# Optimization experiments

Hardware: AMD Instinct MI355X
Metric: run time of the kernel (lower is better)

The kernel has to match this reference:

```python
import jax, jax.numpy as jnp
import numpy as np

NU, NI, K, D, B = 100000, 50000, 100, 64, 8192


def setup_inputs() -> dict:
    key = jax.random.key(0)
    ks = jax.random.split(key, 16)
    s = lambda fan_in: np.sqrt(2.0 / fan_in)  # kaiming_normal-ish scale
    return {
        "user_emb": jax.random.normal(ks[0], (NU, D), jnp.float32) * s(D),
        "item_emb": jax.random.normal(ks[1], (NI, D), jnp.float32) * s(D),
        "user_scr_tensor": jax.random.uniform(ks[2], (NU, K), jnp.float32) / K,
        "item_scr_tensor": jax.random.uniform(ks[3], (NI, K), jnp.float32) / K,
        "w1": jax.random.normal(ks[4], (64, 128), jnp.float32) * s(128),
        "b1": jnp.zeros((64,), jnp.float32),
        "w2": jax.random.normal(ks[5], (64, 64), jnp.float32) * s(64),
        "b2": jnp.zeros((64,), jnp.float32),
        "w3": jax.random.normal(ks[6], (32, 64), jnp.float32) * s(64),
        "b3": jnp.zeros((32,), jnp.float32),
        "w4": jax.random.normal(ks[7], (32, 32), jnp.float32) * s(32),
        "b4": jnp.zeros((32,), jnp.float32),
        "w5": jax.random.normal(ks[8], (1, 32), jnp.float32) * s(32),
        "b5": jnp.zeros((1,), jnp.float32),
        "user_idx_tensor": jax.random.randint(ks[9], (NU, K), 0, NU, jnp.int32),
        "item_idx_tensor": jax.random.randint(ks[10], (NI, K), 0, NI, jnp.int32),
        "user_idxs": jax.random.randint(ks[11], (B,), 0, NU, jnp.int32),
        "item_idxs": jax.random.randint(ks[12], (B,), 0, NI, jnp.int32),
    }


def _scored_pool(idx_tensor, emb, scr, idxs):
    neighs = idx_tensor[idxs]          # [B, K]
    neigh_emb = emb[neighs]            # [B, K, D]
    neigh_scr = scr[neighs]            # [B, K, K]
    return jnp.einsum("bkj,bjd->bkd", neigh_scr, neigh_emb)


def reference(user_emb, item_emb, user_scr_tensor, item_scr_tensor,
              w1, b1, w2, b2, w3, b3, w4, b4, w5, b5,
              user_idx_tensor, item_idx_tensor, user_idxs, item_idxs):
    su = _scored_pool(user_idx_tensor, user_emb, user_scr_tensor, user_idxs)  # [B,K,D]
    si = _scored_pool(item_idx_tensor, item_emb, item_scr_tensor, item_idxs)  # [B,K,D]
    x = jnp.concatenate([su, si], axis=2)  # [B, K, 2D]
    x = jax.nn.relu(x @ w1.T + b1)
    x = jax.nn.relu(x @ w2.T + b2)
    x = jax.nn.relu(x @ w3.T + b3)
    x = jax.nn.relu(x @ w4.T + b4)
    x = jax.nn.sigmoid(x @ w5.T + b5)  # [B, K, 1]
    return jnp.mean(x, axis=-2).squeeze()  # [B]
```

## Files before the change

kernel.cpp:

```cpp
#include <hip/hip_runtime.h>
#include <hip/hip_bf16.h>
#include <math.h>

typedef __attribute__((ext_vector_type(8))) short short8;
typedef __attribute__((ext_vector_type(4))) float f32x4;

#define KN 100

#define W1_OFF 0
#define W2_OFF 8192
#define W3_OFF 12288
#define W4_OFF 14336
#define SCRU_OFF 16384
#define SCRI_OFF (SCRU_OFF + 100000 * 128)
#define EMBU_OFF (SCRI_OFF + 50000 * 128)
#define EMBI_OFF (EMBU_OFF + 100000 * 64)

#define ET_OFF 0
#define XU_OFF (64 * 136)
#define XI_OFF (XU_OFF + 112 * 72)
#define S_TOT  (XI_OFF + 112 * 72)

__device__ __forceinline__ unsigned short f2bf(float f) {
  __hip_bfloat16 h = __float2bfloat16(f);
  return __builtin_bit_cast(unsigned short, h);
}

__device__ __forceinline__ void st8(unsigned short* d, float4 a, float4 b) {
  short8 h;
  h[0] = (short)f2bf(a.x); h[1] = (short)f2bf(a.y);
  h[2] = (short)f2bf(a.z); h[3] = (short)f2bf(a.w);
  h[4] = (short)f2bf(b.x); h[5] = (short)f2bf(b.y);
  h[6] = (short)f2bf(b.z); h[7] = (short)f2bf(b.w);
  *reinterpret_cast<short8*>(d) = h;
}

__global__ void prep(const float* __restrict__ w1, const float* __restrict__ w2,
                     const float* __restrict__ w3, const float* __restrict__ w4,
                     const float* __restrict__ uscr, const float* __restrict__ iscr,
                     const float* __restrict__ uemb, const float* __restrict__ iemb,
                     unsigned short* __restrict__ ws) {
  int t = blockIdx.x * 256 + threadIdx.x;
  if (t < 15360) {
    const float* src; int rel, o, i, kt, base;
    if (t < 8192)       { src = w1; rel = t;         o = rel >> 7; i = rel & 127; kt = 4; base = W1_OFF; }
    else if (t < 12288) { src = w2; rel = t - 8192;  o = rel >> 6; i = rel & 63;  kt = 2; base = W2_OFF; }
    else if (t < 14336) { src = w3; rel = t - 12288; o = rel >> 6; i = rel & 63;  kt = 2; base = W3_OFF; }
    else                { src = w4; rel = t - 14336; o = rel >> 5; i = rel & 31;  kt = 1; base = W4_OFF; }
    int n = o >> 4, l15 = o & 15, k = i >> 5, quad = (i >> 3) & 3, j = i & 7;
    ws[base + ((n * kt + k) * 64 + quad * 16 + l15) * 8 + j] = f2bf(src[rel]);
    return;
  }
  int rel = t - 15360;
  const float4 z4 = {0.f, 0.f, 0.f, 0.f};
  if (rel < 2400000) {
    const float* src; unsigned short* dst; int row, g;
    if (rel < 1600000) {
      row = rel >> 4; g = rel & 15;
      src = uscr + (size_t)row * 100;
      dst = ws + SCRU_OFF + (size_t)row * 128 + g * 8;
    } else {
      int q = rel - 1600000; row = q >> 4; g = q & 15;
      src = iscr + (size_t)row * 100;
      dst = ws + SCRI_OFF + (size_t)row * 128 + g * 8;
    }
    float4 va = (g < 13) ? *reinterpret_cast<const float4*>(src + g * 8) : z4;
    float4 vb = (g < 12) ? *reinterpret_cast<const float4*>(src + g * 8 + 4) : z4;
    st8(dst, va, vb);
    return;
  }
  rel -= 2400000;
  if (rel < 1200000) {
    const float* src; unsigned short* dst; int row, g;
    if (rel < 800000) {
      row = rel >> 3; g = rel & 7;
      src = uemb + (size_t)row * 64;
      dst = ws + EMBU_OFF + (size_t)row * 64 + g * 8;
    } else {
      int q = rel - 800000; row = q >> 3; g = q & 7;
      src = iemb + (size_t)row * 64;
      dst = ws + EMBI_OFF + (size_t)row * 64 + g * 8;
    }
    float4 va = *reinterpret_cast<const float4*>(src + g * 8);
    float4 vb = *reinterpret_cast<const float4*>(src + g * 8 + 4);
    st8(dst, va, vb);
  }
}

template <int NT, int KT, bool RELU>
__device__ __forceinline__ void mlp_layer(const short8* a,
                                          const unsigned short* __restrict__ gw,
                                          const float* __restrict__ bias,
                                          unsigned short* __restrict__ Y, int sY,
                                          int w, int l15, int quad, int lane) {
#pragma unroll
  for (int n = 0; n < NT; ++n) {
    f32x4 acc = {0.f, 0.f, 0.f, 0.f};
#pragma unroll
    for (int k = 0; k < KT; ++k) {
      short8 bf = *reinterpret_cast<const short8*>(gw + ((n * KT + k) * 64 + lane) * 8);
      acc = __builtin_amdgcn_mfma_f32_16x16x32_bf16(a[k], bf, acc, 0, 0, 0);
    }
    const int col = n * 16 + l15;
    const float bv = bias[col];
#pragma unroll
    for (int r = 0; r < 4; ++r) {
      float v = acc[r] + bv;
      if (RELU) v = fmaxf(v, 0.f);
      Y[(w * 16 + quad * 4 + r) * sY + col] = f2bf(v);
    }
  }
}

__launch_bounds__(448)
__global__ void cnn_mfma3(
    const unsigned short* __restrict__ ws,
    const float* __restrict__ b1, const float* __restrict__ b2,
    const float* __restrict__ b3, const float* __restrict__ b4,
    const float* __restrict__ w5, const float* __restrict__ b5,
    const int* __restrict__ user_idx_t, const int* __restrict__ item_idx_t,
    const int* __restrict__ user_idxs, const int* __restrict__ item_idxs,
    float* __restrict__ out) {
  __shared__ __align__(16) unsigned short S[S_TOT];
  __shared__ int s_nb[2][112];
  __shared__ float s_red[7];

  const int b = blockIdx.x;
  const int tid = threadIdx.x;
  const int w = tid >> 6;
  const int lane = tid & 63;
  const int l15 = lane & 15, quad = lane >> 4;

  if (tid < 112) {
    s_nb[0][tid] = (tid < KN) ? user_idx_t[(size_t)user_idxs[b] * KN + tid] : 0;
  } else if (tid >= 128 && tid < 240) {
    int i = tid - 128;
    s_nb[1][i] = (i < KN) ? item_idx_t[(size_t)item_idxs[b] * KN + i] : 0;
  }
  {
    int* z = (int*)S;
    for (int i = tid; i < (64 * 136) / 2; i += 448) z[i] = 0;
  }
  __syncthreads();

  const int mrow = w * 16 + l15;
  const int c = lane & 31, half = lane >> 5;

#pragma unroll 1
  for (int src = 0; src < 2; ++src) {
    const unsigned short* scrb = ws + (src ? SCRI_OFF : SCRU_OFF);
    const unsigned short* embb = ws + (src ? EMBI_OFF : EMBU_OFF);
    const int* nb = s_nb[src];

    short8 a[4];
    {
      const unsigned short* arow = scrb + (size_t)nb[mrow] * 128;
#pragma unroll
      for (int k = 0; k < 4; ++k)
        a[k] = *reinterpret_cast<const short8*>(arow + k * 32 + quad * 8);
    }

#pragma unroll
    for (int rr = 0; rr < 8; ++rr) {
      const int rbase = w + rr * 7;
      if (rbase < 50) {
        const int r = rbase * 2 + half;
        unsigned int v = *reinterpret_cast<const unsigned int*>(
            embb + (size_t)nb[r] * 64 + c * 2);
        S[ET_OFF + (2 * c) * 136 + r] = (unsigned short)(v & 0xffffu);
        S[ET_OFF + (2 * c + 1) * 136 + r] = (unsigned short)(v >> 16);
      }
    }
    __syncthreads();

    const int xoff = src ? XI_OFF : XU_OFF;
#pragma unroll
    for (int n = 0; n < 4; ++n) {
      f32x4 acc = {0.f, 0.f, 0.f, 0.f};
#pragma unroll
      for (int k = 0; k < 4; ++k) {
        short8 bf = *reinterpret_cast<const short8*>(
            S + ET_OFF + (n * 16 + l15) * 136 + k * 32 + quad * 8);
        acc = __builtin_amdgcn_mfma_f32_16x16x32_bf16(a[k], bf, acc, 0, 0, 0);
      }
#pragma unroll
      for (int r = 0; r < 4; ++r)
        S[xoff + (w * 16 + quad * 4 + r) * 72 + n * 16 + l15] = f2bf(acc[r]);
    }
    if (src == 0) __syncthreads();
  }

  {
    short8 a[4];
    a[0] = *reinterpret_cast<const short8*>(S + XU_OFF + (w * 16 + l15) * 72 + quad * 8);
    a[1] = *reinterpret_cast<const short8*>(S + XU_OFF + (w * 16 + l15) * 72 + 32 + quad * 8);
    a[2] = *reinterpret_cast<const short8*>(S + XI_OFF + (w * 16 + l15) * 72 + quad * 8);
    a[3] = *reinterpret_cast<const short8*>(S + XI_OFF + (w * 16 + l15) * 72 + 32 + quad * 8);
    mlp_layer<4, 4, true>(a, ws + W1_OFF, b1, S + XU_OFF, 72, w, l15, quad, lane);
  }
  {
    short8 a[2];
    a[0] = *reinterpret_cast<const short8*>(S + XU_OFF + (w * 16 + l15) * 72 + quad * 8);
    a[1] = *reinterpret_cast<const short8*>(S + XU_OFF + (w * 16 + l15) * 72 + 32 + quad * 8);
    mlp_layer<4, 2, true>(a, ws + W2_OFF, b2, S + XI_OFF, 72, w, l15, quad, lane);
  }
  {
    short8 a[2];
    a[0] = *reinterpret_cast<const short8*>(S + XI_OFF + (w * 16 + l15) * 72 + quad * 8);
    a[1] = *reinterpret_cast<const short8*>(S + XI_OFF + (w * 16 + l15) * 72 + 32 + quad * 8);
    mlp_layer<2, 2, true>(a, ws + W3_OFF, b3, S + XU_OFF, 72, w, l15, quad, lane);
  }
  {
    short8 a = *reinterpret_cast<const short8*>(S + XU_OFF + (w * 16 + l15) * 72 + quad * 8);
    float dot[4] = {0.f, 0.f, 0.f, 0.f};
#pragma unroll
    for (int n = 0; n < 2; ++n) {
      f32x4 acc = {0.f, 0.f, 0.f, 0.f};
      short8 bf = *reinterpret_cast<const short8*>(ws + W4_OFF + (n * 64 + lane) * 8);
      acc = __builtin_amdgcn_mfma_f32_16x16x32_bf16(a, bf, acc, 0, 0, 0);
      const int col = n * 16 + l15;
      const float bv = b4[col], wv = w5[col];
#pragma unroll
      for (int r = 0; r < 4; ++r) {
        float v = fmaxf(acc[r] + bv, 0.f);
        dot[r] = fmaf(v, wv, dot[r]);
      }
    }
    float wsum = 0.f;
    const float bb5 = b5[0];
#pragma unroll
    for (int r = 0; r < 4; ++r) {
      float s = dot[r];
      s += __shfl_xor(s, 1, 64);
      s += __shfl_xor(s, 2, 64);
      s += __shfl_xor(s, 4, 64);
      s += __shfl_xor(s, 8, 64);
      const int row = w * 16 + quad * 4 + r;
      if (l15 == 0 && row < KN) wsum += 1.f / (1.f + expf(-(s + bb5)));
    }
    wsum += __shfl_xor(wsum, 16, 64);
    wsum += __shfl_xor(wsum, 32, 64);
    if (lane == 0) s_red[w] = wsum;
  }
  __syncthreads();
  if (tid == 0) {
    float t = 0.f;
#pragma unroll
    for (int i = 0; i < 7; ++i) t += s_red[i];
    out[b] = t * (1.0f / KN);
  }
}

extern "C" void kernel_launch(void* const* d_in, const int* in_sizes, int n_in,
                              void* d_out, int out_size, void* d_ws,
                              size_t ws_size, hipStream_t stream) {
  const float* user_emb = (const float*)d_in[0];
  const float* item_emb = (const float*)d_in[1];
  const float* user_scr = (const float*)d_in[2];
  const float* item_scr = (const float*)d_in[3];
  const float* w1 = (const float*)d_in[4];
  const float* b1 = (const float*)d_in[5];
  const float* w2 = (const float*)d_in[6];
  const float* b2 = (const float*)d_in[7];
  const float* w3 = (const float*)d_in[8];
  const float* b3 = (const float*)d_in[9];
  const float* w4 = (const float*)d_in[10];
  const float* b4 = (const float*)d_in[11];
  const float* w5 = (const float*)d_in[12];
  const float* b5 = (const float*)d_in[13];
  const int* user_idx_t = (const int*)d_in[14];
  const int* item_idx_t = (const int*)d_in[15];
  const int* user_idxs = (const int*)d_in[16];
  const int* item_idxs = (const int*)d_in[17];
  unsigned short* wsw = (unsigned short*)d_ws;

  prep<<<dim3((15360 + 2400000 + 1200000 + 255) / 256), dim3(256), 0, stream>>>(
      w1, w2, w3, w4, user_scr, item_scr, user_emb, item_emb, wsw);

  const int B = in_sizes[16];
  cnn_mfma3<<<dim3(B), dim3(448), 0, stream>>>(
      wsw, b1, b2, b3, b4, w5, b5, user_idx_t, item_idx_t, user_idxs,
      item_idxs, (float*)d_out);
}
```

Before: 379.2 us.

## Gather embedding operands directly into MFMA registers, dropping LDS transpose staging

Each wave now builds the MFMA B operand for the scored-pool GEMM by gathering eight bf16 values per lane straight from the global embedding table. This replaces staging a transposed embedding tile in shared memory, which needed a zero-fill pass and several block barriers. The intermediate activations are merged into one 112x136 shared buffer whose column halves are reused across MLP layers, and launch bounds now request higher occupancy. The cost is that every wave redundantly issues many small 2-byte scattered global loads, four times per output tile, so the kernel leans much more on cache hit rates.

```diff
diff --git a/kernel.cpp b/kernel.cpp
--- a/kernel.cpp
+++ b/kernel.cpp
@@ -4,6 +4,7 @@
 
 typedef __attribute__((ext_vector_type(8))) short short8;
 typedef __attribute__((ext_vector_type(4))) float f32x4;
+typedef __attribute__((ext_vector_type(4))) unsigned int uint4v;
 
 #define KN 100
 
@@ -16,10 +17,8 @@
 #define EMBU_OFF (SCRI_OFF + 50000 * 128)
 #define EMBI_OFF (EMBU_OFF + 100000 * 64)
 
-#define ET_OFF 0
-#define XU_OFF (64 * 136)
-#define XI_OFF (XU_OFF + 112 * 72)
-#define S_TOT  (XI_OFF + 112 * 72)
+#define XS 136
+#define S_TOT (112 * XS)
 
 __device__ __forceinline__ unsigned short f2bf(float f) {
   __hip_bfloat16 h = __float2bfloat16(f);
@@ -87,11 +86,11 @@
   }
 }
 
-template <int NT, int KT, bool RELU>
+template <int NT, int KT>
 __device__ __forceinline__ void mlp_layer(const short8* a,
                                           const unsigned short* __restrict__ gw,
                                           const float* __restrict__ bias,
-                                          unsigned short* __restrict__ Y, int sY,
+                                          unsigned short* __restrict__ S, int ycol0,
                                           int w, int l15, int quad, int lane) {
 #pragma unroll
   for (int n = 0; n < NT; ++n) {
@@ -105,15 +104,14 @@
     const float bv = bias[col];
 #pragma unroll
     for (int r = 0; r < 4; ++r) {
-      float v = acc[r] + bv;
-      if (RELU) v = fmaxf(v, 0.f);
-      Y[(w * 16 + quad * 4 + r) * sY + col] = f2bf(v);
-    }
-  }
-}
-
-__launch_bounds__(448)
-__global__ void cnn_mfma3(
+      float v = fmaxf(acc[r] + bv, 0.f);
+      S[(w * 16 + quad * 4 + r) * XS + ycol0 + col] = f2bf(v);
+    }
+  }
+}
+
+__launch_bounds__(448, 8)
+__global__ void cnn_mfma4(
     const unsigned short* __restrict__ ws,
     const float* __restrict__ b1, const float* __restrict__ b2,
     const float* __restrict__ b3, const float* __restrict__ b4,
@@ -122,7 +120,7 @@
     const int* __restrict__ user_idxs, const int* __restrict__ item_idxs,
     float* __restrict__ out) {
   __shared__ __align__(16) unsigned short S[S_TOT];
-  __shared__ int s_nb[2][112];
+  __shared__ __align__(16) int s_nb[2][128];
   __shared__ float s_red[7];
 
   const int b = blockIdx.x;
@@ -131,87 +129,75 @@
   const int lane = tid & 63;
   const int l15 = lane & 15, quad = lane >> 4;
 
-  if (tid < 112) {
+  if (tid < 128) {
     s_nb[0][tid] = (tid < KN) ? user_idx_t[(size_t)user_idxs[b] * KN + tid] : 0;
-  } else if (tid >= 128 && tid < 240) {
-    int i = tid - 128;
+  } else if (tid < 256) {
+    const int i = tid - 128;
     s_nb[1][i] = (i < KN) ? item_idx_t[(size_t)item_idxs[b] * KN + i] : 0;
   }
-  {
-    int* z = (int*)S;
-    for (int i = tid; i < (64 * 136) / 2; i += 448) z[i] = 0;
-  }
   __syncthreads();
-
-  const int mrow = w * 16 + l15;
-  const int c = lane & 31, half = lane >> 5;
 
 #pragma unroll 1
   for (int src = 0; src < 2; ++src) {
-    const unsigned short* scrb = ws + (src ? SCRI_OFF : SCRU_OFF);
-    const unsigned short* embb = ws + (src ? EMBI_OFF : EMBU_OFF);
-    const int* nb = s_nb[src];
-
+    const char* scrb = (const char*)(ws + (src ? SCRI_OFF : SCRU_OFF));
+    const char* embb = (const char*)(ws + (src ? EMBI_OFF : EMBU_OFF));
+    const int* nbs = s_nb[src];
+    const unsigned int aoff = (unsigned int)nbs[w * 16 + l15] << 8;
+    const int xc0 = src * 64;
+#pragma unroll
+    for (int nt = 0; nt < 4; ++nt) {
+      const unsigned int dd = (unsigned int)(nt * 16 + l15) * 2;
+      f32x4 acc = {0.f, 0.f, 0.f, 0.f};
+#pragma unroll
+      for (int kt = 0; kt < 4; ++kt) {
+        short8 a = *reinterpret_cast<const short8*>(scrb + aoff + kt * 64 + quad * 16);
+        const int* np = nbs + kt * 32 + quad * 8;
+        const int4 n0 = *reinterpret_cast<const int4*>(np);
+        const int4 n1 = *reinterpret_cast<const int4*>(np + 4);
+        unsigned short h0 = *(const unsigned short*)(embb + (((unsigned int)n0.x << 7) + dd));
+        unsigned short h1 = *(const unsigned short*)(embb + (((unsigned int)n0.y << 7) + dd));
+        unsigned short h2 = *(const unsigned short*)(embb + (((unsigned int)n0.z << 7) + dd));
+        unsigned short h3 = *(const unsigned short*)(embb + (((unsigned int)n0.w << 7) + dd));
+        unsigned short h4 = *(const unsigned short*)(embb + (((unsigned int)n1.x << 7) + dd));
+        unsigned short h5 = *(const unsigned short*)(embb + (((unsigned int)n1.y << 7) + dd));
+        unsigned short h6 = *(const unsigned short*)(embb + (((unsigned int)n1.z << 7) + dd));
+        unsigned short h7 = *(const unsigned short*)(embb + (((unsigned int)n1.w << 7) + dd));
+        uint4v pk;
+        pk.x = (unsigned int)h0 | ((unsigned int)h1 << 16);
+        pk.y = (unsigned int)h2 | ((unsigned int)h3 << 16);
+        pk.z = (unsigned int)h4 | ((unsigned int)h5 << 16);
+        pk.w = (unsigned int)h6 | ((unsigned int)h7 << 16);
+        short8 bf = __builtin_bit_cast(short8, pk);
+        acc = __builtin_amdgcn_mfma_f32_16x16x32_bf16(a, bf, acc, 0, 0, 0);
+      }
+#pragma unroll
+      for (int r = 0; r < 4; ++r)
+        S[(w * 16 + quad * 4 + r) * XS + xc0 + nt * 16 + l15] = f2bf(acc[r]);
+    }
+  }
+
+  const unsigned short* xrow = S + (w * 16 + l15) * XS;
+  {
     short8 a[4];
-    {
-      const unsigned short* arow = scrb + (size_t)nb[mrow] * 128;
-#pragma unroll
-      for (int k = 0; k < 4; ++k)
-        a[k] = *reinterpret_cast<const short8*>(arow + k * 32 + quad * 8);
-    }
-
-#pragma unroll
-    for (int rr = 0; rr < 8; ++rr) {
-      const int rbase = w + rr * 7;
-      if (rbase < 50) {
-        const int r = rbase * 2 + half;
-        unsigned int v = *reinterpret_cast<const unsigned int*>(
-            embb + (size_t)nb[r] * 64 + c * 2);
-        S[ET_OFF + (2 * c) * 136 + r] = (unsigned short)(v & 0xffffu);
-        S[ET_OFF + (2 * c + 1) * 136 + r] = (unsigned short)(v >> 16);
-      }
-    }
-    __syncthreads();
-
-    const int xoff = src ? XI_OFF : XU_OFF;
-#pragma unroll
-    for (int n = 0; n < 4; ++n) {
-      f32x4 acc = {0.f, 0.f, 0.f, 0.f};
-#pragma unroll
-      for (int k = 0; k < 4; ++k) {
-        short8 bf = *reinterpret_cast<const short8*>(
-            S + ET_OFF + (n * 16 + l15) * 136 + k * 32 + quad * 8);
-        acc = __builtin_amdgcn_mfma_f32_16x16x32_bf16(a[k], bf, acc, 0, 0, 0);
-      }
-#pragma unroll
-      for (int r = 0; r < 4; ++r)
-        S[xoff + (w * 16 + quad * 4 + r) * 72 + n * 16 + l15] = f2bf(acc[r]);
-    }
-    if (src == 0) __syncthreads();
-  }
-
-  {
-    short8 a[4];
-    a[0] = *reinterpret_cast<const short8*>(S + XU_OFF + (w * 16 + l15) * 72 + quad * 8);
-    a[1] = *reinterpret_cast<const short8*>(S + XU_OFF + (w * 16 + l15) * 72 + 32 + quad * 8);
-    a[2] = *reinterpret_cast<const short8*>(S + XI_OFF + (w * 16 + l15) * 72 + quad * 8);
-    a[3] = *reinterpret_cast<const short8*>(S + XI_OFF + (w * 16 + l15) * 72 + 32 + quad * 8);
-    mlp_layer<4, 4, true>(a, ws + W1_OFF, b1, S + XU_OFF, 72, w, l15, quad, lane);
+#pragma unroll
+    for (int k = 0; k < 4; ++k)
+      a[k] = *reinterpret_cast<const short8*>(xrow + k * 32 + quad * 8);
+    mlp_layer<4, 4>(a, ws + W1_OFF, b1, S, 0, w, l15, quad, lane);
   }
   {
     short8 a[2];
-    a[0] = *reinterpret_cast<const short8*>(S + XU_OFF + (w * 16 + l15) * 72 + quad * 8);
-    a[1] = *reinterpret_cast<const short8*>(S + XU_OFF + (w * 16 + l15) * 72 + 32 + quad * 8);
-    mlp_layer<4, 2, true>(a, ws + W2_OFF, b2, S + XI_OFF, 72, w, l15, quad, lane);
+    a[0] = *reinterpret_cast<const short8*>(xrow + quad * 8);
+    a[1] = *reinterpret_cast<const short8*>(xrow + 32 + quad * 8);
+    mlp_layer<4, 2>(a, ws + W2_OFF, b2, S, 64, w, l15, quad, lane);
   }
   {
     short8 a[2];
-    a[0] = *reinterpret_cast<const short8*>(S + XI_OFF + (w * 16 + l15) * 72 + quad * 8);
-    a[1] = *reinterpret_cast<const short8*>(S + XI_OFF + (w * 16 + l15) * 72 + 32 + quad * 8);
-    mlp_layer<2, 2, true>(a, ws + W3_OFF, b3, S + XU_OFF, 72, w, l15, quad, lane);
-  }
-  {
-    short8 a = *reinterpret_cast<const short8*>(S + XU_OFF + (w * 16 + l15) * 72 + quad * 8);
+    a[0] = *reinterpret_cast<const short8*>(xrow + 64 + quad * 8);
+    a[1] = *reinterpret_cast<const short8*>(xrow + 96 + quad * 8);
+    mlp_layer<2, 2>(a, ws + W3_OFF, b3, S, 0, w, l15, quad, lane);
+  }
+  {
+    short8 a = *reinterpret_cast<const short8*>(xrow + quad * 8);
     float dot[4] = {0.f, 0.f, 0.f, 0.f};
 #pragma unroll
     for (int n = 0; n < 2; ++n) {
@@ -278,7 +264,7 @@
       w1, w2, w3, w4, user_scr, item_scr, user_emb, item_emb, wsw);
 
   const int B = in_sizes[16];
-  cnn_mfma3<<<dim3(B), dim3(448), 0, stream>>>(
+  cnn_mfma4<<<dim3(B), dim3(448), 0, stream>>>(
       wsw, b1, b2, b3, b4, w5, b5, user_idx_t, item_idx_t, user_idxs,
       item_idxs, (float*)d_out);
 }
```

After: 582.3 us. 53.6% more time.

## Gather neighbour indices in prep and process user/item gathers concurrently

Applied to the files above, without the earlier changes.

Moves the first-level neighbour index gather into the prep kernel, which writes a padded [B,256] index table to the workspace. The main kernel then issues the user and item scr/emb gathers together into two separate transposed LDS buffers, so there is one load phase and one barrier instead of two serialized passes. It also zeroes only the padding columns rather than the whole buffer, and sets a minimum occupancy hint of 6 in launch_bounds. The cost is more registers for the in-flight loads, a larger LDS footprint and extra prep traffic for the index table.

```diff
diff --git a/kernel.cpp b/kernel.cpp
--- a/kernel.cpp
+++ b/kernel.cpp
@@ -15,11 +15,13 @@
 #define SCRI_OFF (SCRU_OFF + 100000 * 128)
 #define EMBU_OFF (SCRI_OFF + 50000 * 128)
 #define EMBI_OFF (EMBU_OFF + 100000 * 64)
-
-#define ET_OFF 0
-#define XU_OFF (64 * 136)
-#define XI_OFF (XU_OFF + 112 * 72)
-#define S_TOT  (XI_OFF + 112 * 72)
+#define NB_OFF   (EMBI_OFF + 50000 * 64)
+
+#define ETU 0
+#define ETI 8704
+#define XU  17408
+#define XI  8704
+#define S_TOT 25472
 
 __device__ __forceinline__ unsigned short f2bf(float f) {
   __hip_bfloat16 h = __float2bfloat16(f);
@@ -39,6 +41,8 @@
                      const float* __restrict__ w3, const float* __restrict__ w4,
                      const float* __restrict__ uscr, const float* __restrict__ iscr,
                      const float* __restrict__ uemb, const float* __restrict__ iemb,
+                     const int* __restrict__ uidx_t, const int* __restrict__ iidx_t,
+                     const int* __restrict__ uidxs, const int* __restrict__ iidxs,
                      unsigned short* __restrict__ ws) {
   int t = blockIdx.x * 256 + threadIdx.x;
   if (t < 15360) {
@@ -84,14 +88,27 @@
     float4 va = *reinterpret_cast<const float4*>(src + g * 8);
     float4 vb = *reinterpret_cast<const float4*>(src + g * 8 + 4);
     st8(dst, va, vb);
-  }
-}
-
-template <int NT, int KT, bool RELU>
+    return;
+  }
+  rel -= 1200000;
+  if (rel < 2097152) {
+    const int b = rel >> 8, i = rel & 255;
+    int v;
+    if (i < 128) {
+      v = (i < KN) ? uidx_t[(size_t)uidxs[b] * KN + i] : 0;
+    } else {
+      const int j = i - 128;
+      v = (j < KN) ? iidx_t[(size_t)iidxs[b] * KN + j] : 0;
+    }
+    ((int*)(ws + NB_OFF))[rel] = v;
+  }
+}
+
+template <int NT, int KT>
 __device__ __forceinline__ void mlp_layer(const short8* a,
                                           const unsigned short* __restrict__ gw,
                                           const float* __restrict__ bias,
-                                          unsigned short* __restrict__ Y, int sY,
+                                          unsigned short* __restrict__ Y,
                                           int w, int l15, int quad, int lane) {
 #pragma unroll
   for (int n = 0; n < NT; ++n) {
@@ -105,24 +122,20 @@
     const float bv = bias[col];
 #pragma unroll
     for (int r = 0; r < 4; ++r) {
-      float v = acc[r] + bv;
-      if (RELU) v = fmaxf(v, 0.f);
-      Y[(w * 16 + quad * 4 + r) * sY + col] = f2bf(v);
-    }
-  }
-}
-
-__launch_bounds__(448)
-__global__ void cnn_mfma3(
+      float v = fmaxf(acc[r] + bv, 0.f);
+      Y[(w * 16 + quad * 4 + r) * 72 + col] = f2bf(v);
+    }
+  }
+}
+
+__launch_bounds__(448, 6)
+__global__ void cnn_mfma5(
     const unsigned short* __restrict__ ws,
     const float* __restrict__ b1, const float* __restrict__ b2,
     const float* __restrict__ b3, const float* __restrict__ b4,
     const float* __restrict__ w5, const float* __restrict__ b5,
-    const int* __restrict__ user_idx_t, const int* __restrict__ item_idx_t,
-    const int* __restrict__ user_idxs, const int* __restrict__ item_idxs,
     float* __restrict__ out) {
   __shared__ __align__(16) unsigned short S[S_TOT];
-  __shared__ int s_nb[2][112];
   __shared__ float s_red[7];
 
   const int b = blockIdx.x;
@@ -130,88 +143,116 @@
   const int w = tid >> 6;
   const int lane = tid & 63;
   const int l15 = lane & 15, quad = lane >> 4;
-
-  if (tid < 112) {
-    s_nb[0][tid] = (tid < KN) ? user_idx_t[(size_t)user_idxs[b] * KN + tid] : 0;
-  } else if (tid >= 128 && tid < 240) {
-    int i = tid - 128;
-    s_nb[1][i] = (i < KN) ? item_idx_t[(size_t)item_idxs[b] * KN + i] : 0;
-  }
-  {
-    int* z = (int*)S;
-    for (int i = tid; i < (64 * 136) / 2; i += 448) z[i] = 0;
+  const int c = lane & 31, half = lane >> 5;
+
+  const int* nbu = (const int*)(ws + NB_OFF) + (size_t)b * 256;
+  const int* nbi = nbu + 128;
+  const char* scru = (const char*)(ws + SCRU_OFF);
+  const char* scri = (const char*)(ws + SCRI_OFF);
+  const char* embu = (const char*)(ws + EMBU_OFF);
+  const char* embi = (const char*)(ws + EMBI_OFF);
+
+  const int mu = nbu[w * 16 + l15];
+  const int mi = nbi[w * 16 + l15];
+
+  short8 au[4], ai[4];
+#pragma unroll
+  for (int k = 0; k < 4; ++k)
+    au[k] = *reinterpret_cast<const short8*>(scru + ((size_t)(unsigned)mu << 8) + k * 64 + quad * 16);
+#pragma unroll
+  for (int k = 0; k < 4; ++k)
+    ai[k] = *reinterpret_cast<const short8*>(scri + ((size_t)(unsigned)mi << 8) + k * 64 + quad * 16);
+
+  unsigned int du[8], di[8];
+  int rv[8];
+#pragma unroll
+  for (int rr = 0; rr < 8; ++rr) {
+    const int rbase = w + rr * 7;
+    if (rbase < 50) {
+      const int r = rbase * 2 + half;
+      rv[rr] = r;
+      du[rr] = *reinterpret_cast<const unsigned int*>(
+          embu + ((size_t)(unsigned)nbu[r] << 7) + c * 4);
+      di[rr] = *reinterpret_cast<const unsigned int*>(
+          embi + ((size_t)(unsigned)nbi[r] << 7) + c * 4);
+    }
+  }
+  for (int q = tid; q < 1792; q += 448) {
+    const int buf = q / 896, rem = q - buf * 896;
+    const int row = rem / 14, cp = rem - row * 14;
+    *reinterpret_cast<unsigned int*>(&S[buf * 8704 + row * 136 + 100 + cp * 2]) = 0u;
+  }
+#pragma unroll
+  for (int rr = 0; rr < 8; ++rr) {
+    const int rbase = w + rr * 7;
+    if (rbase < 50) {
+      const int r = rv[rr];
+      S[ETU + (2 * c) * 136 + r] = (unsigned short)(du[rr] & 0xffffu);
+      S[ETU + (2 * c + 1) * 136 + r] = (unsigned short)(du[rr] >> 16);
+      S[ETI + (2 * c) * 136 + r] = (unsigned short)(di[rr] & 0xffffu);
+      S[ETI + (2 * c + 1) * 136 + r] = (unsigned short)(di[rr] >> 16);
+    }
   }
   __syncthreads();
 
-  const int mrow = w * 16 + l15;
-  const int c = lane & 31, half = lane >> 5;
-
-#pragma unroll 1
-  for (int src = 0; src < 2; ++src) {
-    const unsigned short* scrb = ws + (src ? SCRI_OFF : SCRU_OFF);
-    const unsigned short* embb = ws + (src ? EMBI_OFF : EMBU_OFF);
-    const int* nb = s_nb[src];
-
-    short8 a[4];
-    {
-      const unsigned short* arow = scrb + (size_t)nb[mrow] * 128;
-#pragma unroll
-      for (int k = 0; k < 4; ++k)
-        a[k] = *reinterpret_cast<const short8*>(arow + k * 32 + quad * 8);
-    }
-
-#pragma unroll
-    for (int rr = 0; rr < 8; ++rr) {
-      const int rbase = w + rr * 7;
-      if (rbase < 50) {
-        const int r = rbase * 2 + half;
-        unsigned int v = *reinterpret_cast<const unsigned int*>(
-            embb + (size_t)nb[r] * 64 + c * 2);
-        S[ET_OFF + (2 * c) * 136 + r] = (unsigned short)(v & 0xffffu);
-        S[ET_OFF + (2 * c + 1) * 136 + r] = (unsigned short)(v >> 16);
-      }
-    }
-    __syncthreads();
-
-    const int xoff = src ? XI_OFF : XU_OFF;
-#pragma unroll
-    for (int n = 0; n < 4; ++n) {
-      f32x4 acc = {0.f, 0.f, 0.f, 0.f};
-#pragma unroll
-      for (int k = 0; k < 4; ++k) {
-        short8 bf = *reinterpret_cast<const short8*>(
-            S + ET_OFF + (n * 16 + l15) * 136 + k * 32 + quad * 8);
-        acc = __builtin_amdgcn_mfma_f32_16x16x32_bf16(a[k], bf, acc, 0, 0, 0);
-      }
-#pragma unroll
-      for (int r = 0; r < 4; ++r)
-        S[xoff + (w * 16 + quad * 4 + r) * 72 + n * 16 + l15] = f2bf(acc[r]);
-    }
-    if (src == 0) __syncthreads();
-  }
-
+#pragma unroll
+  for (int nt = 0; nt < 4; ++nt) {
+    f32x4 acc = {0.f, 0.f, 0.f, 0.f};
+#pragma unroll
+    for (int kt = 0; kt < 4; ++kt) {
+      short8 bf = *reinterpret_cast<const short8*>(
+          S + ETU + (nt * 16 + l15) * 136 + kt * 32 + quad * 8);
+      acc = __builtin_amdgcn_mfma_f32_16x16x32_bf16(au[kt], bf, acc, 0, 0, 0);
+    }
+#pragma unroll
+    for (int r = 0; r < 4; ++r)
+      S[XU + (w * 16 + quad * 4 + r) * 72 + nt * 16 + l15] = f2bf(acc[r]);
+  }
+
+  f32x4 acci[4];
+#pragma unroll
+  for (int nt = 0; nt < 4; ++nt) {
+    f32x4 acc = {0.f, 0.f, 0.f, 0.f};
+#pragma unroll
+    for (int kt = 0; kt < 4; ++kt) {
+      short8 bf = *reinterpret_cast<const short8*>(
+          S + ETI + (nt * 16 + l15) * 136 + kt * 32 + quad * 8);
+      acc = __builtin_amdgcn_mfma_f32_16x16x32_bf16(ai[kt], bf, acc, 0, 0, 0);
+    }
+    acci[nt] = acc;
+  }
+  __syncthreads();
+
+#pragma unroll
+  for (int nt = 0; nt < 4; ++nt)
+#pragma unroll
+    for (int r = 0; r < 4; ++r)
+      S[XI + (w * 16 + quad * 4 + r) * 72 + nt * 16 + l15] = f2bf(acci[nt][r]);
+
+  const unsigned short* xu_row = S + XU + (w * 16 + l15) * 72;
+  const unsigned short* xi_row = S + XI + (w * 16 + l15) * 72;
   {
     short8 a[4];
-    a[0] = *reinterpret_cast<const short8*>(S + XU_OFF + (w * 16 + l15) * 72 + quad * 8);
-    a[1] = *reinterpret_cast<const short8*>(S + XU_OFF + (w * 16 + l15) * 72 + 32 + quad * 8);
-    a[2] = *reinterpret_cast<const short8*>(S + XI_OFF + (w * 16 + l15) * 72 + quad * 8);
-    a[3] = *reinterpret_cast<const short8*>(S + XI_OFF + (w * 16 + l15) * 72 + 32 + quad * 8);
-    mlp_layer<4, 4, true>(a, ws + W1_OFF, b1, S + XU_OFF, 72, w, l15, quad, lane);
+    a[0] = *reinterpret_cast<const short8*>(xu_row + quad * 8);
+    a[1] = *reinterpret_cast<const short8*>(xu_row + 32 + quad * 8);
+    a[2] = *reinterpret_cast<const short8*>(xi_row + quad * 8);
+    a[3] = *reinterpret_cast<const short8*>(xi_row + 32 + quad * 8);
+    mlp_layer<4, 4>(a, ws + W1_OFF, b1, S + XU, w, l15, quad, lane);
   }
   {
     short8 a[2];
-    a[0] = *reinterpret_cast<const short8*>(S + XU_OFF + (w * 16 + l15) * 72 + quad * 8);
-    a[1] = *reinterpret_cast<const short8*>(S + XU_OFF + (w * 16 + l15) * 72 + 32 + quad * 8);
-    mlp_layer<4, 2, true>(a, ws + W2_OFF, b2, S + XI_OFF, 72, w, l15, quad, lane);
+    a[0] = *reinterpret_cast<const short8*>(xu_row + quad * 8);
+    a[1] = *reinterpret_cast<const short8*>(xu_row + 32 + quad * 8);
+    mlp_layer<4, 2>(a, ws + W2_OFF, b2, S + XI, w, l15, quad, lane);
   }
   {
     short8 a[2];
-    a[0] = *reinterpret_cast<const short8*>(S + XI_OFF + (w * 16 + l15) * 72 + quad * 8);
-    a[1] = *reinterpret_cast<const short8*>(S + XI_OFF + (w * 16 + l15) * 72 + 32 + quad * 8);
-    mlp_layer<2, 2, true>(a, ws + W3_OFF, b3, S + XU_OFF, 72, w, l15, quad, lane);
+    a[0] = *reinterpret_cast<const short8*>(xi_row + quad * 8);
+    a[1] = *reinterpret_cast<const short8*>(xi_row + 32 + quad * 8);
+    mlp_layer<2, 2>(a, ws + W3_OFF, b3, S + XU, w, l15, quad, lane);
   }
   {
-    short8 a = *reinterpret_cast<const short8*>(S + XU_OFF + (w * 16 + l15) * 72 + quad * 8);
+    short8 a = *reinterpret_cast<const short8*>(xu_row + quad * 8);
     float dot[4] = {0.f, 0.f, 0.f, 0.f};
 #pragma unroll
     for (int n = 0; n < 2; ++n) {
@@ -274,11 +315,12 @@
   const int* item_idxs = (const int*)d_in[17];
   unsigned short* wsw = (unsigned short*)d_ws;
 
-  prep<<<dim3((15360 + 2400000 + 1200000 + 255) / 256), dim3(256), 0, stream>>>(
-      w1, w2, w3, w4, user_scr, item_scr, user_emb, item_emb, wsw);
+  const int prep_threads = 15360 + 2400000 + 1200000 + 2097152;
+  prep<<<dim3((prep_threads + 255) / 256), dim3(256), 0, stream>>>(
+      w1, w2, w3, w4, user_scr, item_scr, user_emb, item_emb,
+      user_idx_t, item_idx_t, user_idxs, item_idxs, wsw);
 
   const int B = in_sizes[16];
-  cnn_mfma3<<<dim3(B), dim3(448), 0, stream>>>(
-      wsw, b1, b2, b3, b4, w5, b5, user_idx_t, item_idx_t, user_idxs,
-      item_idxs, (float*)d_out);
-}
+  cnn_mfma5<<<dim3(B), dim3(448), 0, stream>>>(
+      wsw, b1, b2, b3, b4, w5, b5, (float*)d_out);
+}
```

Result: slower. 401.6 us (+5.9%).
